# Kernel tuning notes

Hardware: AMD Instinct MI355X
Metric: run time of the kernel (lower is better)

The kernel has to match this reference:

```python
import jax, jax.numpy as jnp
import numpy as np

MUL = 32          # multiplicity of 0e and 1o in edge_messages_irreps
E = 40000         # number of edges
NODE_DIM = 128    # 128x0e node feats
EDGE_DIM = 32     # 32x0e edge feats
WEIGHT_NUMEL = 5 * MUL * MUL  # 5 uvu instructions, (u,v)=(32,32) weights each

# Levi-Civita tensor = sqrt(6) * wigner_3j(1,1,1) in the e3nn real basis
_eps = np.zeros((3, 3, 3), np.float32)
for a, b, c in [(0, 1, 2), (1, 2, 0), (2, 0, 1)]:
    _eps[a, b, c] = 1.0
    _eps[a, c, b] = -1.0
EPS = jnp.asarray(_eps)


def setup_inputs() -> dict:
    key = jax.random.key(0)
    ks = jax.random.split(key, 13)
    return {
        "edge_feats": jax.random.normal(ks[0], (E, EDGE_DIM), jnp.float32),
        "edge_messages1": jax.random.normal(ks[1], (E, 4 * MUL), jnp.float32),
        "edge_messages2": jax.random.normal(ks[2], (E, 4 * MUL), jnp.float32),
        "node_feats_sender": jax.random.normal(ks[3], (E, NODE_DIM), jnp.float32),
        "node_feats_receiver": jax.random.normal(ks[4], (E, NODE_DIM), jnp.float32),
        "W_nodes": jax.random.normal(ks[5], (NODE_DIM, EDGE_DIM), jnp.float32),
        "W_mlp1": jax.random.normal(ks[6], (3 * EDGE_DIM, 128), jnp.float32),
        "W_mlp2": jax.random.normal(ks[7], (128, 128), jnp.float32),
        "W_mlp3": jax.random.normal(ks[8], (128, WEIGHT_NUMEL), jnp.float32),
        "W_out_0e": jax.random.normal(ks[9], (2 * MUL, MUL), jnp.float32),
        "W_out_1o": jax.random.normal(ks[10], (2 * MUL, MUL), jnp.float32),
        "W_out_1e": jax.random.normal(ks[11], (MUL, MUL), jnp.float32),
        "edge_index": jax.random.randint(ks[12], (2, E), 0, 10000, jnp.int64 if jax.config.jax_enable_x64 else jnp.int32),
    }


def reference(edge_feats, edge_messages1, edge_messages2, node_feats_sender,
              node_feats_receiver, W_nodes, W_mlp1, W_mlp2, W_mlp3,
              W_out_0e, W_out_1o, W_out_1e, edge_index):
    # nodes_linear: o3.Linear on pure scalars == dense matmul with 1/sqrt(fan_in)
    s_send = (node_feats_sender @ W_nodes) * (1.0 / np.sqrt(NODE_DIM))
    s_recv = (node_feats_receiver @ W_nodes) * (1.0 / np.sqrt(NODE_DIM))
    scal = jnp.concatenate([s_send, s_recv, edge_feats], axis=1)  # [E, 96]

    # FullyConnectedNet [96,128,128,weight_numel] with SiLU, e3nn fan-in scaling
    h = jax.nn.silu((scal @ W_mlp1) * (1.0 / np.sqrt(3 * EDGE_DIM)))
    h = jax.nn.silu((h @ W_mlp2) * (1.0 / np.sqrt(128)))
    w = (h @ W_mlp3) * (1.0 / np.sqrt(128))          # [E, 5120] per-edge TP weights
    w = w.reshape(-1, 5, MUL, MUL)                    # 5 uvu instructions

    # split messages into 32x0e scalars and 32x1o vectors
    x1_0 = edge_messages1[:, :MUL]
    x1_1 = edge_messages1[:, MUL:].reshape(-1, MUL, 3)
    x2_0 = edge_messages2[:, :MUL]
    x2_1 = edge_messages2[:, MUL:].reshape(-1, MUL, 3)

    # per-edge-weighted uvu tensor product; alpha = sqrt(ir_out.dim / fan) with
    # CG constants (1, d/sqrt(3), eps/sqrt(6)) folded in
    c1 = jnp.einsum('euv,eu,ev->eu', w[:, 0], x1_0, x2_0) * (1.0 / np.sqrt(MUL))          # 0e
    c2 = jnp.einsum('euv,eu,evj->euj', w[:, 1], x1_0, x2_1) * (1.0 / np.sqrt(MUL))        # 1o
    c3 = jnp.einsum('euv,eui,ev->eui', w[:, 2], x1_1, x2_0) * (1.0 / np.sqrt(MUL))        # 1o
    c4 = jnp.einsum('euv,eui,evi->eu', w[:, 3], x1_1, x2_1) * (1.0 / np.sqrt(3 * MUL))    # 0e
    c5 = jnp.einsum('euv,eui,evj,ijk->euk', w[:, 4], x1_1, x2_1, EPS) * (1.0 / np.sqrt(2 * MUL))  # 1e

    # output_linear: o3.Linear over irreps_mid -> 32x0e + 32x1o + 32x1e
    mid_0e = jnp.concatenate([c1, c4], axis=1)        # [E, 64]
    mid_1o = jnp.concatenate([c2, c3], axis=1)        # [E, 64, 3]
    out_0e = (mid_0e @ W_out_0e) * (1.0 / np.sqrt(2 * MUL))                      # [E, 32]
    out_1o = jnp.einsum('euj,uw->ewj', mid_1o, W_out_1o) * (1.0 / np.sqrt(2 * MUL))
    out_1e = jnp.einsum('euk,uw->ewk', c5, W_out_1e) * (1.0 / np.sqrt(MUL))

    n = out_0e.shape[0]
    return jnp.concatenate(
        [out_0e, out_1o.reshape(n, 3 * MUL), out_1e.reshape(n, 3 * MUL)], axis=1)  # [E, 224]
```

## Files before the change

### kernel.cpp

```cpp
#include <hip/hip_runtime.h>
#include <hip/hip_bf16.h>
#include <math.h>

typedef __attribute__((ext_vector_type(8)))  short bf16x8;
typedef __attribute__((ext_vector_type(4)))  float f32x4;
typedef __attribute__((ext_vector_type(16))) float f32x16;

#define S128 0.08838834764831845f
#define S96  0.10206207261596575f
#define S32  0.17677669529663687f
#define S64  0.125f

__device__ __forceinline__ float silu_f(float x){ return x / (1.0f + expf(-x)); }
__device__ __forceinline__ ushort f2b(float x){
    __hip_bfloat16 b = __float2bfloat16(x); return *(ushort*)&b;
}
__device__ __forceinline__ float b2f(ushort u){
    return __uint_as_float(((uint)u) << 16);
}
__device__ __forceinline__ float blo(uint d){ return __uint_as_float(d << 16); }
__device__ __forceinline__ float bhi(uint d){ return __uint_as_float(d & 0xffff0000u); }
__device__ __forceinline__ uint packbf(float a, float b){
    return (uint)f2b(a) | ((uint)f2b(b) << 16);
}

__global__ __launch_bounds__(256)
void prep_weights(const float* __restrict__ Wn, const float* __restrict__ W1,
                  const float* __restrict__ W2, ushort* __restrict__ WnT,
                  ushort* __restrict__ W1T, ushort* __restrict__ W2T) {
    int idx = blockIdx.x * 256 + threadIdx.x;
    if (idx < 4096) {
        int n = idx >> 7, k = idx & 127;
        WnT[n * 128 + k] = f2b(Wn[k * 32 + n]);
    } else if (idx < 16384) {
        int t = idx - 4096; int n = t / 96, k = t - n * 96;
        W1T[n * 96 + k] = f2b(W1[k * 128 + n]);
    } else {
        int t = idx - 16384; int n = t >> 7, k = t & 127;
        W2T[n * 128 + k] = f2b(W2[k * 128 + n]);
    }
}

__global__ __launch_bounds__(256)
void w3_fragpack(const float* __restrict__ W3, ushort* __restrict__ w3A) {
    const int pu = blockIdx.x;
    const int t  = threadIdx.x;
    #pragma unroll
    for (int s = 0; s < 2; ++s) {
        int slot = s * 256 + t;
        int ks = slot >> 6, l = slot & 63;
        int m = pu * 32 + (l & 31);
        int kbase = ks * 16 + (l >> 5) * 8;
        bf16x8 v;
        #pragma unroll
        for (int i = 0; i < 8; ++i)
            v[i] = (short)f2b(W3[(size_t)(kbase + i) * 5120 + m]);
        *(bf16x8*)&w3A[((size_t)(pu * 8 + ks) * 64 + l) * 8] = v;
    }
}

__global__ __launch_bounds__(512, 2)
void mega(const float* __restrict__ ef,  const float* __restrict__ em1,
          const float* __restrict__ em2, const float* __restrict__ nfs,
          const float* __restrict__ nfr, const ushort* __restrict__ WnT,
          const ushort* __restrict__ W1T, const ushort* __restrict__ W2T,
          const ushort* __restrict__ w3A, const float* __restrict__ W0e,
          const float* __restrict__ W1o, const float* __restrict__ W1e,
          float* __restrict__ out)
{
    __shared__ __align__(16) ushort dlds[64 * 362];
    __shared__ __align__(16) ushort hbuf[64 * 132];
    __shared__ __align__(16) uint   xp2[2 * 64 * 34];

    const int tid  = threadIdx.x;
    const int lane = tid & 63, wv = tid >> 6;
    const int l15  = lane & 15, lg = lane >> 4;
    const int e0   = blockIdx.x * 64;

    ushort* scal = dlds;
    ushort* h1b  = dlds + 6656;
    float*  x2f  = (float*)dlds;

    #pragma unroll
    for (int q = 0; q < 4; ++q) {
        int idx = q * 512 + tid;
        int e = idx >> 5, c4 = idx & 31;
        float4 v = *(const float4*)(em2 + (size_t)(e0 + e) * 128 + c4 * 4);
        *(float4*)&x2f[e * 132 + c4 * 4] = v;
    }
    __syncthreads();

    {
        int part = tid >> 7;
        int sub  = tid & 127;
        int e = sub >> 1, hi2 = sub & 1;
        const float* xr = &x2f[e * 132];
        uint* dst = &xp2[(hi2 * 64 + e) * 34];
        if (part == 0) {
            #pragma unroll
            for (int g = 0; g < 4; ++g)
                #pragma unroll
                for (int c = 0; c < 2; ++c) {
                    int v0 = 8 * g + 4 * hi2 + 2 * c;
                    dst[g * 2 + c] = packbf(xr[v0], xr[v0 + 1]);
                }
        } else {
            int j = part - 1;
            #pragma unroll
            for (int g = 0; g < 4; ++g)
                #pragma unroll
                for (int c = 0; c < 2; ++c) {
                    int v0 = 8 * g + 4 * hi2 + 2 * c;
                    dst[8 + j * 8 + g * 2 + c] =
                        packbf(xr[32 + v0 * 3 + j], xr[32 + (v0 + 1) * 3 + j]);
                }
        }
    }
    __syncthreads();

    #pragma unroll
    for (int q = 0; q < 4; ++q) {
        int idx = q * 512 + tid;
        int e = idx >> 5, j = idx & 31;
        scal[e * 104 + 64 + j] = f2b(ef[(size_t)(e0 + e) * 32 + j]);
    }

    {
        const int h = wv >> 2, eb = (wv & 3) * 16;
        const float* src = h ? nfr : nfs;
        const size_t erow = (size_t)(e0 + eb + l15) * 128;
        f32x4 acc1[2] = {{0,0,0,0},{0,0,0,0}};
        #pragma unroll
        for (int ks = 0; ks < 4; ++ks) {
            float4 va = *(const float4*)(src + erow + ks * 32 + lg * 8);
            float4 vb = *(const float4*)(src + erow + ks * 32 + lg * 8 + 4);
            bf16x8 a;
            a[0]=(short)f2b(va.x); a[1]=(short)f2b(va.y);
            a[2]=(short)f2b(va.z); a[3]=(short)f2b(va.w);
            a[4]=(short)f2b(vb.x); a[5]=(short)f2b(vb.y);
            a[6]=(short)f2b(vb.z); a[7]=(short)f2b(vb.w);
            #pragma unroll
            for (int nf = 0; nf < 2; ++nf) {
                bf16x8 b = *(const bf16x8*)(WnT + (nf * 16 + l15) * 128 + ks * 32 + lg * 8);
                acc1[nf] = __builtin_amdgcn_mfma_f32_16x16x32_bf16(a, b, acc1[nf], 0, 0, 0);
            }
        }
        #pragma unroll
        for (int nf = 0; nf < 2; ++nf)
            #pragma unroll
            for (int r = 0; r < 4; ++r)
                scal[(eb + lg * 4 + r) * 104 + h * 32 + nf * 16 + l15] =
                    f2b(acc1[nf][r] * S128);
    }
    __syncthreads();

    {
        const int et = wv & 3, nh = wv >> 2;
        f32x4 acc2[4] = {{0,0,0,0},{0,0,0,0},{0,0,0,0},{0,0,0,0}};
        #pragma unroll
        for (int ks = 0; ks < 3; ++ks) {
            bf16x8 a = *(const bf16x8*)&scal[(et * 16 + l15) * 104 + ks * 32 + lg * 8];
            #pragma unroll
            for (int nf = 0; nf < 4; ++nf) {
                int gn = nh * 4 + nf;
                bf16x8 b = *(const bf16x8*)(W1T + (gn * 16 + l15) * 96 + ks * 32 + lg * 8);
                acc2[nf] = __builtin_amdgcn_mfma_f32_16x16x32_bf16(a, b, acc2[nf], 0, 0, 0);
            }
        }
        #pragma unroll
        for (int nf = 0; nf < 4; ++nf)
            #pragma unroll
            for (int r = 0; r < 4; ++r)
                h1b[(et * 16 + lg * 4 + r) * 136 + (nh * 4 + nf) * 16 + l15] =
                    f2b(silu_f(acc2[nf][r] * S96));
    }
    __syncthreads();

    {
        const int et = wv & 3, nh = wv >> 2;
        f32x4 acc3[4] = {{0,0,0,0},{0,0,0,0},{0,0,0,0},{0,0,0,0}};
        #pragma unroll
        for (int ks = 0; ks < 4; ++ks) {
            bf16x8 a = *(const bf16x8*)&h1b[(et * 16 + l15) * 136 + ks * 32 + lg * 8];
            #pragma unroll
            for (int nf = 0; nf < 4; ++nf) {
                int gn = nh * 4 + nf;
                bf16x8 b = *(const bf16x8*)(W2T + (gn * 16 + l15) * 128 + ks * 32 + lg * 8);
                acc3[nf] = __builtin_amdgcn_mfma_f32_16x16x32_bf16(a, b, acc3[nf], 0, 0, 0);
            }
        }
        #pragma unroll
        for (int nf = 0; nf < 4; ++nf)
            #pragma unroll
            for (int r = 0; r < 4; ++r) {
                int e = et * 16 + lg * 4 + r;
                int col = (nh * 4 + nf) * 16 + l15;
                hbuf[e * 128 + (col ^ ((e & 15) << 3))] =
                    f2b(silu_f(acc3[nf][r] * S128));
            }
    }
    __syncthreads();

    const int el = lane & 31;
    const int hi = lane >> 5;
    const int ew = hi * 32 + el;
    const uint* xb0 = &xp2[(hi * 64 + el) * 34];
    const uint* xb1 = &xp2[(hi * 64 + 32 + el) * 34];
    ushort* drow = &dlds[ew * 362];
    const int k0 = hi * 8;
    const int sw0 = (el & 15) << 3;

    #pragma unroll 1
    for (int un = 0; un < 20; ++un) {
        const int pu = wv * 20 + un;
        const int p = pu >> 5, u = pu & 31;

        bf16x8 a[8];
        const ushort* Ab = w3A + ((size_t)pu * 8 * 64 + lane) * 8;
        #pragma unroll
        for (int ks = 0; ks < 8; ++ks)
            a[ks] = *(const bf16x8*)(Ab + (size_t)ks * 512);

        f32x16 acc0 = {0,0,0,0,0,0,0,0,0,0,0,0,0,0,0,0};
        f32x16 acc1 = {0,0,0,0,0,0,0,0,0,0,0,0,0,0,0,0};
        #pragma unroll
        for (int ks = 0; ks < 8; ++ks) {
            int ko = (ks * 16 + k0) ^ sw0;
            bf16x8 b0 = *(const bf16x8*)&hbuf[el * 128 + ko];
            bf16x8 b1 = *(const bf16x8*)&hbuf[(32 + el) * 128 + ko];
            acc0 = __builtin_amdgcn_mfma_f32_32x32x16_bf16(a[ks], b0, acc0, 0, 0, 0);
            acc1 = __builtin_amdgcn_mfma_f32_32x32x16_bf16(a[ks], b1, acc1, 0, 0, 0);
        }

        if (p == 0 || p == 2) {
            const int off = (p == 0) ? 0 : 128;
            float s0 = 0.f, s1 = 0.f;
            #pragma unroll
            for (int g = 0; g < 4; ++g) {
                uint2 q0 = *(const uint2*)&xb0[g * 2];
                uint2 q1 = *(const uint2*)&xb1[g * 2];
                s0 += acc0[g*4+0]*blo(q0.x) + acc0[g*4+1]*bhi(q0.x)
                    + acc0[g*4+2]*blo(q0.y) + acc0[g*4+3]*bhi(q0.y);
                s1 += acc1[g*4+0]*blo(q1.x) + acc1[g*4+1]*bhi(q1.x)
                    + acc1[g*4+2]*blo(q1.y) + acc1[g*4+3]*bhi(q1.y);
            }
            s0 += __shfl_xor(s0, 32);
            s1 += __shfl_xor(s1, 32);
            drow[off + u] = f2b((hi ? s1 : s0) * S128);
        } else {
            const int off = ((p == 1) ? 32 : (p == 3) ? 160 : 256) + u * 3;
            #pragma unroll
            for (int j = 0; j < 3; ++j) {
                float s0 = 0.f, s1 = 0.f;
                #pragma unroll
                for (int g = 0; g < 4; ++g) {
                    uint2 q0 = *(const uint2*)&xb0[8 + j * 8 + g * 2];
                    uint2 q1 = *(const uint2*)&xb1[8 + j * 8 + g * 2];
                    s0 += acc0[g*4+0]*blo(q0.x) + acc0[g*4+1]*bhi(q0.x)
                        + acc0[g*4+2]*blo(q0.y) + acc0[g*4+3]*bhi(q0.y);
                    s1 += acc1[g*4+0]*blo(q1.x) + acc1[g*4+1]*bhi(q1.x)
                        + acc1[g*4+2]*blo(q1.y) + acc1[g*4+3]*bhi(q1.y);
                }
                s0 += __shfl_xor(s0, 32);
                s1 += __shfl_xor(s1, 32);
                drow[off + j] = f2b((hi ? s1 : s0) * S128);
            }
        }
    }
    __syncthreads();

    {
        int e = tid >> 3, seg = tid & 7;
        const float* x1 = em1 + (size_t)(e0 + e) * 128 + seg * 16;
        #pragma unroll
        for (int q = 0; q < 4; ++q) {
            float4 v = *(const float4*)(x1 + q * 4);
            *(uint*)&hbuf[e * 132 + seg * 16 + q * 4]     = packbf(v.x, v.y);
            *(uint*)&hbuf[e * 132 + seg * 16 + q * 4 + 2] = packbf(v.z, v.w);
        }
    }
    __syncthreads();

    #pragma unroll 1
    for (int it = 0; it < 4; ++it) {
        int unit = wv + 8 * it;
        if (unit >= 28) break;
        int mi = unit & 3, task = unit >> 2;
        int e = mi * 16 + l15;
        const ushort* de = &dlds[e * 362];
        const ushort* xe = &hbuf[e * 132];
        const size_t orow = (size_t)(e0 + mi * 16 + lg * 4) * 224;

        if (task == 0) {
            bf16x8 af0, af1;
            #pragma unroll
            for (int t = 0; t < 8; ++t) {
                int u = lg * 8 + t;
                af0[t] = (short)f2b(S32 * b2f(xe[u]) * b2f(de[u]));
                float c4 = 0.f;
                #pragma unroll
                for (int i = 0; i < 3; ++i)
                    c4 += b2f(xe[32 + u * 3 + i]) * b2f(de[160 + u * 3 + i]);
                af1[t] = (short)f2b(c4 * S96);
            }
            #pragma unroll
            for (int nf = 0; nf < 2; ++nf) {
                bf16x8 bf0, bf1;
                #pragma unroll
                for (int t = 0; t < 8; ++t) {
                    bf0[t] = (short)f2b(W0e[(lg * 8 + t) * 32 + nf * 16 + l15]);
                    bf1[t] = (short)f2b(W0e[(32 + lg * 8 + t) * 32 + nf * 16 + l15]);
                }
                f32x4 o = {0.f, 0.f, 0.f, 0.f};
                o = __builtin_amdgcn_mfma_f32_16x16x32_bf16(af0, bf0, o, 0, 0, 0);
                o = __builtin_amdgcn_mfma_f32_16x16x32_bf16(af1, bf1, o, 0, 0, 0);
                #pragma unroll
                for (int rr = 0; rr < 4; ++rr)
                    out[orow + (size_t)rr * 224 + nf * 16 + l15] = o[rr] * S64;
            }
        } else if (task <= 3) {
            int j = task - 1;
            bf16x8 af0, af1;
            #pragma unroll
            for (int t = 0; t < 8; ++t) {
                int u = lg * 8 + t;
                af0[t] = (short)f2b(S32 * b2f(xe[u]) * b2f(de[32 + u * 3 + j]));
                af1[t] = (short)f2b(S32 * b2f(xe[32 + u * 3 + j]) * b2f(de[128 + u]));
            }
            #pragma unroll
            for (int nf = 0; nf < 2; ++nf) {
                bf16x8 bf0, bf1;
                #pragma unroll
                for (int t = 0; t < 8; ++t) {
                    bf0[t] = (short)f2b(W1o[(lg * 8 + t) * 32 + nf * 16 + l15]);
                    bf1[t] = (short)f2b(W1o[(32 + lg * 8 + t) * 32 + nf * 16 + l15]);
                }
                f32x4 o = {0.f, 0.f, 0.f, 0.f};
                o = __builtin_amdgcn_mfma_f32_16x16x32_bf16(af0, bf0, o, 0, 0, 0);
                o = __builtin_amdgcn_mfma_f32_16x16x32_bf16(af1, bf1, o, 0, 0, 0);
                #pragma unroll
                for (int rr = 0; rr < 4; ++rr)
                    out[orow + (size_t)rr * 224 + 32 + (nf * 16 + l15) * 3 + j] = o[rr] * S64;
            }
        } else {
            int k = task - 4;
            int k1 = k + 1; if (k1 > 2) k1 -= 3;
            int k2 = k + 2; if (k2 > 2) k2 -= 3;
            bf16x8 af0;
            #pragma unroll
            for (int t = 0; t < 8; ++t) {
                int u = lg * 8 + t;
                float a_ = b2f(xe[32 + u * 3 + k1]) * b2f(de[256 + u * 3 + k2])
                         - b2f(xe[32 + u * 3 + k2]) * b2f(de[256 + u * 3 + k1]);
                af0[t] = (short)f2b(a_ * S64);
            }
            #pragma unroll
            for (int nf = 0; nf < 2; ++nf) {
                bf16x8 bf0;
                #pragma unroll
                for (int t = 0; t < 8; ++t)
                    bf0[t] = (short)f2b(W1e[(lg * 8 + t) * 32 + nf * 16 + l15]);
                f32x4 o = {0.f, 0.f, 0.f, 0.f};
                o = __builtin_amdgcn_mfma_f32_16x16x32_bf16(af0, bf0, o, 0, 0, 0);
                #pragma unroll
                for (int rr = 0; rr < 4; ++rr)
                    out[orow + (size_t)rr * 224 + 128 + (nf * 16 + l15) * 3 + k] = o[rr] * S32;
            }
        }
    }
}

extern "C" void kernel_launch(void* const* d_in, const int* in_sizes, int n_in,
                              void* d_out, int out_size, void* d_ws, size_t ws_size,
                              hipStream_t stream) {
    const float* ef  = (const float*)d_in[0];
    const float* em1 = (const float*)d_in[1];
    const float* em2 = (const float*)d_in[2];
    const float* nfs = (const float*)d_in[3];
    const float* nfr = (const float*)d_in[4];
    const float* Wn  = (const float*)d_in[5];
    const float* W1  = (const float*)d_in[6];
    const float* W2  = (const float*)d_in[7];
    const float* W3  = (const float*)d_in[8];
    const float* W0e = (const float*)d_in[9];
    const float* W1o = (const float*)d_in[10];
    const float* W1e = (const float*)d_in[11];
    float* out = (float*)d_out;

    const int E = in_sizes[0] / 32;

    char* ws = (char*)d_ws;
    ushort* w3A = (ushort*)ws;
    size_t off = (size_t)5120 * 128 * 2;
    ushort* WnT = (ushort*)(ws + off);  off += 32 * 128 * 2;
    ushort* W1T = (ushort*)(ws + off);  off += 128 * 96 * 2;
    ushort* W2T = (ushort*)(ws + off);

    prep_weights<<<128, 256, 0, stream>>>(Wn, W1, W2, WnT, W1T, W2T);
    w3_fragpack<<<160, 256, 0, stream>>>(W3, w3A);
    mega<<<E / 64, 512, 0, stream>>>(ef, em1, em2, nfs, nfr,
                                     WnT, W1T, W2T, w3A, W0e, W1o, W1e, out);
}
```

Measured before the change: 168.2 us.

## Split mega kernel into MLP+contraction and finalize kernels via global intermediate

The fused kernel is split in two. The first kernel runs the MLP and the weight-contraction stage with a smaller LDS footprint and a higher occupancy hint, and writes a transposed bf16 intermediate of shape [352, E] to workspace. A second kernel reads it back, applies the em1 products and the output linear, and writes the result. The aim is higher occupancy by freeing the large per-block LDS buffer, with edge halves processed sequentially to cut accumulator registers. The cost is an extra global round trip (~28 MB bf16), a second launch, and the hardcoded E constant NE.

```diff
diff --git a/kernel.cpp b/kernel.cpp
--- a/kernel.cpp
+++ b/kernel.cpp
@@ -10,6 +10,7 @@
 #define S96  0.10206207261596575f
 #define S32  0.17677669529663687f
 #define S64  0.125f
+#define NE   40000
 
 __device__ __forceinline__ float silu_f(float x){ return x / (1.0f + expf(-x)); }
 __device__ __forceinline__ ushort f2b(float x){
@@ -59,64 +60,24 @@
     }
 }
 
-__global__ __launch_bounds__(512, 2)
-void mega(const float* __restrict__ ef,  const float* __restrict__ em1,
-          const float* __restrict__ em2, const float* __restrict__ nfs,
-          const float* __restrict__ nfr, const ushort* __restrict__ WnT,
-          const ushort* __restrict__ W1T, const ushort* __restrict__ W2T,
-          const ushort* __restrict__ w3A, const float* __restrict__ W0e,
-          const float* __restrict__ W1o, const float* __restrict__ W1e,
-          float* __restrict__ out)
+__global__ __launch_bounds__(512, 6)
+void mega2(const float* __restrict__ ef,  const float* __restrict__ em2,
+           const float* __restrict__ nfs, const float* __restrict__ nfr,
+           const ushort* __restrict__ WnT, const ushort* __restrict__ W1T,
+           const ushort* __restrict__ W2T, const ushort* __restrict__ w3A,
+           ushort* __restrict__ dt)
 {
-    __shared__ __align__(16) ushort dlds[64 * 362];
-    __shared__ __align__(16) ushort hbuf[64 * 132];
-    __shared__ __align__(16) uint   xp2[2 * 64 * 34];
+    __shared__ __align__(16) ushort scratch[15360];
+    __shared__ __align__(16) ushort hbuf[64 * 128];
 
     const int tid  = threadIdx.x;
     const int lane = tid & 63, wv = tid >> 6;
     const int l15  = lane & 15, lg = lane >> 4;
     const int e0   = blockIdx.x * 64;
 
-    ushort* scal = dlds;
-    ushort* h1b  = dlds + 6656;
-    float*  x2f  = (float*)dlds;
-
-    #pragma unroll
-    for (int q = 0; q < 4; ++q) {
-        int idx = q * 512 + tid;
-        int e = idx >> 5, c4 = idx & 31;
-        float4 v = *(const float4*)(em2 + (size_t)(e0 + e) * 128 + c4 * 4);
-        *(float4*)&x2f[e * 132 + c4 * 4] = v;
-    }
-    __syncthreads();
-
-    {
-        int part = tid >> 7;
-        int sub  = tid & 127;
-        int e = sub >> 1, hi2 = sub & 1;
-        const float* xr = &x2f[e * 132];
-        uint* dst = &xp2[(hi2 * 64 + e) * 34];
-        if (part == 0) {
-            #pragma unroll
-            for (int g = 0; g < 4; ++g)
-                #pragma unroll
-                for (int c = 0; c < 2; ++c) {
-                    int v0 = 8 * g + 4 * hi2 + 2 * c;
-                    dst[g * 2 + c] = packbf(xr[v0], xr[v0 + 1]);
-                }
-        } else {
-            int j = part - 1;
-            #pragma unroll
-            for (int g = 0; g < 4; ++g)
-                #pragma unroll
-                for (int c = 0; c < 2; ++c) {
-                    int v0 = 8 * g + 4 * hi2 + 2 * c;
-                    dst[8 + j * 8 + g * 2 + c] =
-                        packbf(xr[32 + v0 * 3 + j], xr[32 + (v0 + 1) * 3 + j]);
-                }
-        }
-    }
-    __syncthreads();
+    ushort* scal = scratch;
+    ushort* h1b  = scratch + 6656;
+    uint*   xp2  = (uint*)scratch;
 
     #pragma unroll
     for (int q = 0; q < 4; ++q) {
@@ -189,6 +150,7 @@
                 acc3[nf] = __builtin_amdgcn_mfma_f32_16x16x32_bf16(a, b, acc3[nf], 0, 0, 0);
             }
         }
+        __syncthreads();
         #pragma unroll
         for (int nf = 0; nf < 4; ++nf)
             #pragma unroll
@@ -199,108 +161,146 @@
                     f2b(silu_f(acc3[nf][r] * S128));
             }
     }
+
+    {
+        int part = tid >> 7;
+        int sub  = tid & 127;
+        int e = sub >> 1, hi2 = sub & 1;
+        const float* xr = em2 + (size_t)(e0 + e) * 128;
+        uint* dst = &xp2[(hi2 * 64 + e) * 34];
+        if (part == 0) {
+            #pragma unroll
+            for (int g = 0; g < 4; ++g)
+                #pragma unroll
+                for (int c = 0; c < 2; ++c) {
+                    int v0 = 8 * g + 4 * hi2 + 2 * c;
+                    float2 t1 = *(const float2*)(xr + v0);
+                    dst[g * 2 + c] = packbf(t1.x, t1.y);
+                }
+        } else {
+            int j = part - 1;
+            #pragma unroll
+            for (int g = 0; g < 4; ++g)
+                #pragma unroll
+                for (int c = 0; c < 2; ++c) {
+                    int v0 = 8 * g + 4 * hi2 + 2 * c;
+                    dst[8 + j * 8 + g * 2 + c] =
+                        packbf(xr[32 + v0 * 3 + j], xr[32 + (v0 + 1) * 3 + j]);
+                }
+        }
+    }
     __syncthreads();
 
-    const int el = lane & 31;
-    const int hi = lane >> 5;
-    const int ew = hi * 32 + el;
-    const uint* xb0 = &xp2[(hi * 64 + el) * 34];
-    const uint* xb1 = &xp2[(hi * 64 + 32 + el) * 34];
-    ushort* drow = &dlds[ew * 362];
-    const int k0 = hi * 8;
+    const int el  = lane & 31;
+    const int hi  = lane >> 5;
     const int sw0 = (el & 15) << 3;
 
     #pragma unroll 1
     for (int un = 0; un < 20; ++un) {
-        const int pu = wv * 20 + un;
+        const int pu = un * 8 + wv;
         const int p = pu >> 5, u = pu & 31;
+        const ushort* Ab = w3A + (size_t)pu * 4096 + lane * 8;
 
         bf16x8 a[8];
-        const ushort* Ab = w3A + ((size_t)pu * 8 * 64 + lane) * 8;
         #pragma unroll
         for (int ks = 0; ks < 8; ++ks)
-            a[ks] = *(const bf16x8*)(Ab + (size_t)ks * 512);
-
-        f32x16 acc0 = {0,0,0,0,0,0,0,0,0,0,0,0,0,0,0,0};
-        f32x16 acc1 = {0,0,0,0,0,0,0,0,0,0,0,0,0,0,0,0};
-        #pragma unroll
-        for (int ks = 0; ks < 8; ++ks) {
-            int ko = (ks * 16 + k0) ^ sw0;
-            bf16x8 b0 = *(const bf16x8*)&hbuf[el * 128 + ko];
-            bf16x8 b1 = *(const bf16x8*)&hbuf[(32 + el) * 128 + ko];
-            acc0 = __builtin_amdgcn_mfma_f32_32x32x16_bf16(a[ks], b0, acc0, 0, 0, 0);
-            acc1 = __builtin_amdgcn_mfma_f32_32x32x16_bf16(a[ks], b1, acc1, 0, 0, 0);
-        }
-
-        if (p == 0 || p == 2) {
-            const int off = (p == 0) ? 0 : 128;
-            float s0 = 0.f, s1 = 0.f;
-            #pragma unroll
-            for (int g = 0; g < 4; ++g) {
-                uint2 q0 = *(const uint2*)&xb0[g * 2];
-                uint2 q1 = *(const uint2*)&xb1[g * 2];
-                s0 += acc0[g*4+0]*blo(q0.x) + acc0[g*4+1]*bhi(q0.x)
-                    + acc0[g*4+2]*blo(q0.y) + acc0[g*4+3]*bhi(q0.y);
-                s1 += acc1[g*4+0]*blo(q1.x) + acc1[g*4+1]*bhi(q1.x)
-                    + acc1[g*4+2]*blo(q1.y) + acc1[g*4+3]*bhi(q1.y);
-            }
-            s0 += __shfl_xor(s0, 32);
-            s1 += __shfl_xor(s1, 32);
-            drow[off + u] = f2b((hi ? s1 : s0) * S128);
-        } else {
-            const int off = ((p == 1) ? 32 : (p == 3) ? 160 : 256) + u * 3;
-            #pragma unroll
-            for (int j = 0; j < 3; ++j) {
-                float s0 = 0.f, s1 = 0.f;
+            a[ks] = *(const bf16x8*)(Ab + ks * 512);
+
+        #pragma unroll 1
+        for (int eh = 0; eh < 2; ++eh) {
+            const int ebase = e0 + eh * 32;
+            const ushort* hrow = &hbuf[(eh * 32 + el) * 128];
+            f32x16 acc = {0,0,0,0,0,0,0,0,0,0,0,0,0,0,0,0};
+            #pragma unroll
+            for (int ks = 0; ks < 8; ++ks) {
+                bf16x8 b = *(const bf16x8*)&hrow[(ks * 16 + hi * 8) ^ sw0];
+                acc = __builtin_amdgcn_mfma_f32_32x32x16_bf16(a[ks], b, acc, 0, 0, 0);
+            }
+            const uint* xb = &xp2[(hi * 64 + eh * 32 + el) * 34];
+            if (p == 0 || p == 2) {
+                const int row = ((p == 0) ? 0 : 128) + u;
+                float s = 0.f;
                 #pragma unroll
                 for (int g = 0; g < 4; ++g) {
-                    uint2 q0 = *(const uint2*)&xb0[8 + j * 8 + g * 2];
-                    uint2 q1 = *(const uint2*)&xb1[8 + j * 8 + g * 2];
-                    s0 += acc0[g*4+0]*blo(q0.x) + acc0[g*4+1]*bhi(q0.x)
-                        + acc0[g*4+2]*blo(q0.y) + acc0[g*4+3]*bhi(q0.y);
-                    s1 += acc1[g*4+0]*blo(q1.x) + acc1[g*4+1]*bhi(q1.x)
-                        + acc1[g*4+2]*blo(q1.y) + acc1[g*4+3]*bhi(q1.y);
-                }
-                s0 += __shfl_xor(s0, 32);
-                s1 += __shfl_xor(s1, 32);
-                drow[off + j] = f2b((hi ? s1 : s0) * S128);
-            }
-        }
-    }
-    __syncthreads();
-
+                    uint2 q = *(const uint2*)&xb[g * 2];
+                    s += acc[g*4+0]*blo(q.x) + acc[g*4+1]*bhi(q.x)
+                       + acc[g*4+2]*blo(q.y) + acc[g*4+3]*bhi(q.y);
+                }
+                s += __shfl_xor(s, 32);
+                if (hi == 0)
+                    dt[(size_t)row * NE + ebase + el] = f2b(s * S128);
+            } else {
+                const int row0 = ((p == 1) ? 32 : (p == 3) ? 160 : 256) + u * 3;
+                float sj[3];
+                #pragma unroll
+                for (int j = 0; j < 3; ++j) {
+                    float s = 0.f;
+                    #pragma unroll
+                    for (int g = 0; g < 4; ++g) {
+                        uint2 q = *(const uint2*)&xb[8 + j * 8 + g * 2];
+                        s += acc[g*4+0]*blo(q.x) + acc[g*4+1]*bhi(q.x)
+                           + acc[g*4+2]*blo(q.y) + acc[g*4+3]*bhi(q.y);
+                    }
+                    s += __shfl_xor(s, 32);
+                    sj[j] = s;
+                }
+                if (hi == 0) {
+                    #pragma unroll
+                    for (int j = 0; j < 3; ++j)
+                        dt[(size_t)(row0 + j) * NE + ebase + el] = f2b(sj[j] * S128);
+                }
+            }
+        }
+    }
+}
+
+__global__ __launch_bounds__(256)
+void finalize2(const float* __restrict__ em1, const ushort* __restrict__ dt,
+               const float* __restrict__ W0e, const float* __restrict__ W1o,
+               const float* __restrict__ W1e, float* __restrict__ out)
+{
+    __shared__ __align__(16) ushort dl[352 * 33];
+    __shared__ __align__(16) ushort x1b[32 * 132];
+    const int tid  = threadIdx.x;
+    const int lane = tid & 63, wv = tid >> 6;
+    const int l15  = lane & 15, lg = lane >> 4;
+    const int eb   = blockIdx.x * 32;
+
+    for (int idx = tid; idx < 352 * 32; idx += 256) {
+        int row = idx >> 5, e = idx & 31;
+        dl[row * 33 + e] = dt[(size_t)row * NE + eb + e];
+    }
     {
         int e = tid >> 3, seg = tid & 7;
-        const float* x1 = em1 + (size_t)(e0 + e) * 128 + seg * 16;
+        const float* x1 = em1 + (size_t)(eb + e) * 128 + seg * 16;
         #pragma unroll
         for (int q = 0; q < 4; ++q) {
             float4 v = *(const float4*)(x1 + q * 4);
-            *(uint*)&hbuf[e * 132 + seg * 16 + q * 4]     = packbf(v.x, v.y);
-            *(uint*)&hbuf[e * 132 + seg * 16 + q * 4 + 2] = packbf(v.z, v.w);
+            *(uint*)&x1b[e * 132 + seg * 16 + q * 4]     = packbf(v.x, v.y);
+            *(uint*)&x1b[e * 132 + seg * 16 + q * 4 + 2] = packbf(v.z, v.w);
         }
     }
     __syncthreads();
 
     #pragma unroll 1
     for (int it = 0; it < 4; ++it) {
-        int unit = wv + 8 * it;
-        if (unit >= 28) break;
-        int mi = unit & 3, task = unit >> 2;
-        int e = mi * 16 + l15;
-        const ushort* de = &dlds[e * 362];
-        const ushort* xe = &hbuf[e * 132];
-        const size_t orow = (size_t)(e0 + mi * 16 + lg * 4) * 224;
+        int unit = it * 4 + wv;
+        if (unit >= 14) break;
+        int mi = unit & 1, task = unit >> 1;
+        const int ei = mi * 16 + l15;
+        const ushort* xe = &x1b[ei * 132];
+        const size_t orow = (size_t)(eb + mi * 16 + lg * 4) * 224;
 
         if (task == 0) {
             bf16x8 af0, af1;
             #pragma unroll
             for (int t = 0; t < 8; ++t) {
                 int u = lg * 8 + t;
-                af0[t] = (short)f2b(S32 * b2f(xe[u]) * b2f(de[u]));
+                af0[t] = (short)f2b(S32 * b2f(xe[u]) * b2f(dl[u * 33 + ei]));
                 float c4 = 0.f;
                 #pragma unroll
                 for (int i = 0; i < 3; ++i)
-                    c4 += b2f(xe[32 + u * 3 + i]) * b2f(de[160 + u * 3 + i]);
+                    c4 += b2f(xe[32 + u * 3 + i]) * b2f(dl[(160 + u * 3 + i) * 33 + ei]);
                 af1[t] = (short)f2b(c4 * S96);
             }
             #pragma unroll
@@ -324,8 +324,8 @@
             #pragma unroll
             for (int t = 0; t < 8; ++t) {
                 int u = lg * 8 + t;
-                af0[t] = (short)f2b(S32 * b2f(xe[u]) * b2f(de[32 + u * 3 + j]));
-                af1[t] = (short)f2b(S32 * b2f(xe[32 + u * 3 + j]) * b2f(de[128 + u]));
+                af0[t] = (short)f2b(S32 * b2f(xe[u]) * b2f(dl[(32 + u * 3 + j) * 33 + ei]));
+                af1[t] = (short)f2b(S32 * b2f(xe[32 + u * 3 + j]) * b2f(dl[(128 + u) * 33 + ei]));
             }
             #pragma unroll
             for (int nf = 0; nf < 2; ++nf) {
@@ -350,8 +350,8 @@
             #pragma unroll
             for (int t = 0; t < 8; ++t) {
                 int u = lg * 8 + t;
-                float a_ = b2f(xe[32 + u * 3 + k1]) * b2f(de[256 + u * 3 + k2])
-                         - b2f(xe[32 + u * 3 + k2]) * b2f(de[256 + u * 3 + k1]);
+                float a_ = b2f(xe[32 + u * 3 + k1]) * b2f(dl[(256 + u * 3 + k2) * 33 + ei])
+                         - b2f(xe[32 + u * 3 + k2]) * b2f(dl[(256 + u * 3 + k1) * 33 + ei]);
                 af0[t] = (short)f2b(a_ * S64);
             }
             #pragma unroll
@@ -394,10 +394,12 @@
     size_t off = (size_t)5120 * 128 * 2;
     ushort* WnT = (ushort*)(ws + off);  off += 32 * 128 * 2;
     ushort* W1T = (ushort*)(ws + off);  off += 128 * 96 * 2;
-    ushort* W2T = (ushort*)(ws + off);
+    ushort* W2T = (ushort*)(ws + off);  off += 128 * 128 * 2;
+    ushort* dt  = (ushort*)(ws + off);
 
     prep_weights<<<128, 256, 0, stream>>>(Wn, W1, W2, WnT, W1T, W2T);
     w3_fragpack<<<160, 256, 0, stream>>>(W3, w3A);
-    mega<<<E / 64, 512, 0, stream>>>(ef, em1, em2, nfs, nfr,
-                                     WnT, W1T, W2T, w3A, W0e, W1o, W1e, out);
-}
+    mega2<<<E / 64, 512, 0, stream>>>(ef, em2, nfs, nfr,
+                                      WnT, W1T, W2T, w3A, dt);
+    finalize2<<<E / 32, 256, 0, stream>>>(em1, dt, W0e, W1o, W1e, out);
+}
```

Result: faster. 152.1 us (-9.5%).
